# Optimization experiments

Hardware: AMD Instinct MI355X
Metric: run time of the kernel (lower is better)

The kernel has to match this reference:

```python
import jax, jax.numpy as jnp
import numpy as np

# PSLoss constants (from init_kwargs)
MSE_WEIGHT = 0.5
W_CORR = 1.0
W_VAR = 1.0
W_MEAN = 1.0
K = 3           # k_dominant_freqs
MIN_PATCH = 5   # min_patch_len (max(2, 5))
EPS = 1e-8


def setup_inputs() -> dict:
    key = jax.random.key(0)
    k1, k2 = jax.random.split(key)
    B, T, F = 64, 336, 321
    forecast = jax.random.normal(k1, (B, T, F), dtype=jnp.float32)
    target = jax.random.normal(k2, (B, T, F), dtype=jnp.float32)
    return {"forecast": forecast, "target": target}


def _structural_loss(fc, tg):
    """fc, tg: [N, T] flattened (batch*features) series. Returns (total_loss_sum, patch_count)."""
    N, T = tg.shape
    Mmax = T // MIN_PATCH  # max segments per period (period >= MIN_PATCH)

    # --- Fourier adaptive patching (vectorized over all N series) ---
    amp = jnp.abs(jnp.fft.rfft(tg, axis=-1))[:, 1:]           # drop DC, [N, T//2]
    _, rel = jax.lax.top_k(amp, K)                             # [N, K]
    freq_idx = (rel + 1).astype(jnp.float32)
    p = jnp.floor(T / freq_idx).astype(jnp.int32)              # dominant periods [N, K]
    # dedup periods in topk order (the original 'processed_periods' set)
    eq = p[:, :, None] == p[:, None, :]                        # [N, K, K]
    earlier = jnp.tril(jnp.ones((K, K), dtype=bool), -1)       # j < k
    dup = jnp.any(eq & earlier, axis=-1)
    valid_p = (p >= MIN_PATCH) & ~dup                          # [N, K]

    nseg = T // p                                              # [N, K] (p >= 2 always)
    s_idx = jnp.arange(Mmax, dtype=jnp.int32)
    seg_s = p[:, :, None] * s_idx                              # [N, K, Mmax]
    seg_e = seg_s + p[:, :, None]
    seg_v = (s_idx < nseg[:, :, None]) & valid_p[:, :, None]
    rem_s = nseg * p                                           # remaining tail patch
    rem_v = valid_p & ((T - rem_s) >= MIN_PATCH)

    starts = jnp.concatenate([seg_s.reshape(N, -1), rem_s], axis=-1)
    ends = jnp.concatenate([seg_e.reshape(N, -1), jnp.full_like(rem_s, T)], axis=-1)
    valid = jnp.concatenate([seg_v.reshape(N, -1), rem_v], axis=-1)
    # fallback whole-series patch if no patch survived
    none = ~jnp.any(valid, axis=-1, keepdims=True)
    starts = jnp.concatenate([starts, jnp.zeros((N, 1), jnp.int32)], axis=-1)
    ends = jnp.concatenate([ends, jnp.full((N, 1), T, jnp.int32)], axis=-1)
    valid = jnp.concatenate([valid, none], axis=-1)            # [N, M]

    # --- dedup identical (start, end) patches (original list(set(...))) ---
    SENT = (T + 1) * (T + 1)
    keys = jnp.where(valid, starts * (T + 1) + ends, SENT)
    keys = jnp.sort(keys, axis=-1)
    uniq = jnp.concatenate(
        [jnp.ones((N, 1), dtype=bool), keys[:, 1:] != keys[:, :-1]], axis=-1)
    valid = (keys != SENT) & uniq
    s = jnp.where(valid, keys // (T + 1), 0)                   # safe dummy (0,2) when invalid
    e = jnp.where(valid, keys % (T + 1), 2)

    # --- per-patch stats via inclusive prefix sums ---
    def csum(x):
        return jnp.concatenate([jnp.zeros((N, 1), x.dtype), jnp.cumsum(x, axis=-1)], axis=-1)

    cs_t, cs_f = csum(tg), csum(fc)
    cs_tt, cs_ff, cs_tf = csum(tg * tg), csum(fc * fc), csum(tg * fc)

    def seg_sum(cs):
        return jnp.take_along_axis(cs, e, axis=-1) - jnp.take_along_axis(cs, s, axis=-1)

    n = (e - s).astype(jnp.float32)
    St, Sf = seg_sum(cs_t), seg_sum(cs_f)
    Stt, Sff, Stf = seg_sum(cs_tt), seg_sum(cs_ff), seg_sum(cs_tf)
    mt, mf = St / n, Sf / n
    tvs = jnp.maximum(Stt - n * mt * mt, 0.0)   # sum of squared deviations (target)
    fvs = jnp.maximum(Sff - n * mf * mf, 0.0)
    num = Stf - n * mt * mf
    corr = num / (jnp.sqrt(tvs * fvs) + EPS)
    corr_loss = 1.0 - jnp.abs(corr)
    tvar = tvs / (n - 1.0)                      # torch.var is unbiased
    fvar = fvs / (n - 1.0)
    var_loss = jnp.abs(tvar - fvar) / (tvar + EPS)
    mean_loss = jnp.abs(mt - mf) / (jnp.abs(mt) + EPS)
    patch_loss = W_CORR * corr_loss + W_VAR * var_loss + W_MEAN * mean_loss

    total = jnp.sum(jnp.where(valid, patch_loss, 0.0))
    count = jnp.sum(valid)
    return total, count


def reference(forecast, target):
    B, T, F = forecast.shape
    fc = jnp.transpose(forecast, (0, 2, 1)).reshape(B * F, T)
    tg = jnp.transpose(target, (0, 2, 1)).reshape(B * F, T)
    total, count = _structural_loss(fc, tg)
    avg = jnp.where(count > 0,
                    total / jnp.maximum(count, 1).astype(jnp.float32),
                    jnp.float32(0.0))
    mse = jnp.mean((forecast - target) ** 2)
    return MSE_WEIGHT * mse + (1.0 - MSE_WEIGHT) * avg
```

## Files before the change

kernel.cpp:

```cpp
#include <hip/hip_runtime.h>
#include <hip/hip_bf16.h>

#define TT 336
#define NF 321
#define NB 64
#define NSER (NB * NF)
#define WPB 4
#define KP 352
#define LDA 360
#define SPP 16
#define WV 8
#define NFB (NSER / SPP)
#define NFBG 1288
#define TSP 340

#define TWS 1056

#define TGX 11
#define TGY 11
#define NMSEP (TGX * TGY * NB)

typedef __attribute__((ext_vector_type(8))) short bf16x8;
typedef __attribute__((ext_vector_type(4))) float f32x4;
typedef unsigned long long ULL;

__device__ __forceinline__ unsigned short f2bf(float v) {
    unsigned x = __float_as_uint(v);
    x += 0x7FFFu + ((x >> 16) & 1u);
    return (unsigned short)(x >> 16);
}

__device__ __forceinline__ void ins3(ULL& a0, ULL& a1, ULL& a2, ULL x) {
    ULL hi = a0 > x ? a0 : x;
    ULL lo = a0 > x ? x : a0;
    a0 = hi;
    ULL hi1 = a1 > lo ? a1 : lo;
    ULL lo1 = a1 > lo ? lo : a1;
    a1 = hi1;
    a2 = a2 > lo1 ? a2 : lo1;
}

__device__ __forceinline__ int idiv336(int d) {
    return (int)(__fdividef(336.0f, (float)d));
}

__global__ void twiddle_k(unsigned short* __restrict__ Wb) {
    int n = blockIdx.x;
    int f = (n >> 1) + 1;
    int isSin = n & 1;
    for (int k = threadIdx.x; k < KP; k += blockDim.x) {
        float v = 0.0f;
        if (k < TT) {
            int r = (f * k) % TT;
            float ang = 6.2831853071795864769f * (float)r / 336.0f;
            v = isSin ? sinf(ang) : cosf(ang);
        }
        Wb[(size_t)n * KP + k] = f2bf(v);
    }
}

__device__ __forceinline__ float patch_loss_f32(float S1, float S2, float S3,
                                                float S4, float S5, int n) {
    float nnf = (float)n;
    float invf = 1.0f / nnf;
    float tvs = S3 - S1 * S1 * invf; tvs = tvs > 0.f ? tvs : 0.f;
    float fvs = S4 - S2 * S2 * invf; fvs = fvs > 0.f ? fvs : 0.f;
    float num = S5 - S1 * S2 * invf;
    float corr = num / (sqrtf(tvs * fvs) + 1e-8f);
    float closs = 1.0f - fabsf(corr);
    float vloss = fabsf(tvs - fvs) / (tvs + (nnf - 1.0f) * 1e-8f);
    float mloss = fabsf(S1 - S2) / (fabsf(S1) + nnf * 1e-8f);
    return closs + vloss + mloss;
}

__device__ __forceinline__ double patch_loss(double S1, double S2, double S3,
                                             double S4, double S5, double nn) {
    double mt = S1 / nn, mf = S2 / nn;
    double tvs = S3 - nn * mt * mt; tvs = tvs > 0.0 ? tvs : 0.0;
    double fvs = S4 - nn * mf * mf; fvs = fvs > 0.0 ? fvs : 0.0;
    double num = S5 - nn * mt * mf;
    double corr = num / (sqrt(tvs * fvs) + 1e-8);
    double closs = 1.0 - fabs(corr);
    double tvar = tvs / (nn - 1.0), fvar = fvs / (nn - 1.0);
    double vloss = fabs(tvar - fvar) / (tvar + 1e-8);
    double mloss = fabs(mt - mf) / (fabs(mt) + 1e-8);
    return closs + vloss + mloss;
}

struct PatchCfg {
    int P[3], nseg[3], rs[3];
    float rp[3];
    bool vp[3], hr[3];
};

__device__ __forceinline__ void make_cfg(int fr0, int fr1, int fr2, PatchCfg& c) {
    c.P[0] = idiv336(fr0); c.P[1] = idiv336(fr1); c.P[2] = idiv336(fr2);
    c.vp[0] = (c.P[0] >= 5);
    c.vp[1] = (c.P[1] >= 5) && (c.P[1] != c.P[0]);
    c.vp[2] = (c.P[2] >= 5) && (c.P[2] != c.P[0]) && (c.P[2] != c.P[1]);
#pragma unroll
    for (int q = 0; q < 3; q++) {
        c.nseg[q] = idiv336(c.P[q] > 0 ? c.P[q] : 1);
        c.rs[q] = c.nseg[q] * c.P[q];
        c.hr[q] = c.vp[q] && ((TT - c.rs[q]) >= 5);
        c.rp[q] = (c.P[q] > 0) ? __frcp_rn((float)c.P[q]) : 0.0f;
    }
}

__device__ __forceinline__ bool slot_patch(const PatchCfg& c, int i, int& s, int& e) {
    bool kept = false;
    s = 0; e = 0;
    if (i < 204) {
        int k = (i >= 136) ? 2 : ((i >= 68) ? 1 : 0);
        int si = i - k * 68;
        if (c.vp[k]) {
            if (si < c.nseg[k]) { s = c.P[k] * si; e = s + c.P[k]; kept = true; }
            else if (si == c.nseg[k] && c.hr[k]) { s = c.rs[k]; e = TT; kept = true; }
            if (kept) {
#pragma unroll
                for (int j = 0; j < 2; j++) {
                    if (j < k && c.vp[j]) {
                        bool dup = (s == c.rs[j]) && (e == TT) && c.hr[j];
                        int len = e - s;
                        if (len == c.P[j] && s < c.rs[j] && (s % c.P[j]) == 0) dup = true;
                        if (dup) kept = false;
                    }
                }
            }
        }
    }
    return kept;
}

__global__ __launch_bounds__(512) void fused_k(const float* __restrict__ tgO,
                                               const float* __restrict__ fcO,
                                               const unsigned short* __restrict__ Wb,
                                               double* __restrict__ blkout) {
    __shared__ __align__(16) char smem[43520 + WV * TWS * 4];
    float2* ts = (float2*)smem;
    unsigned short* sA = (unsigned short*)(smem + 43520);
    ULL* tk3 = (ULL*)(smem + 43520 + 11520);
    float* tabAll = (float*)(smem + 43520);
    __shared__ uint4 tkf[SPP];
    __shared__ double wms[WV], wls[WV];
    __shared__ int wlc[WV];

    const int tid = threadIdx.x;
    const int wave = tid >> 6, lane = tid & 63;
    const int lb = (blockIdx.x & 7) * 161 + (blockIdx.x >> 3);
    if (lb >= NFB) return;
    const int serBase = lb * SPP;

    const int j = tid & 15, tch = tid >> 4;
    int t0, nT;
    if (tch < 16) { t0 = tch * 11; nT = 11; }
    else          { t0 = 176 + (tch - 16) * 10; nT = 10; }
    float va[11], vc[11];
    {
        const int ser = serBase + j;
        const int bb = ser / NF, ff = ser - bb * NF;
        const float* tb_ = tgO + (size_t)bb * TT * NF + ff;
        const float* fb_ = fcO + (size_t)bb * TT * NF + ff;
#pragma unroll
        for (int i = 0; i < 11; i++) if (i < nT) va[i] = tb_[(size_t)(t0 + i) * NF];
#pragma unroll
        for (int i = 0; i < 11; i++) if (i < nT) vc[i] = fb_[(size_t)(t0 + i) * NF];
#pragma unroll
        for (int i = 0; i < 11; i++) {
            if (i < nT) sA[j * LDA + (t0 + i)] = f2bf(va[i]);
        }
        if (tid < SPP * 16) sA[(tid & 15) * LDA + TT + (tid >> 4)] = 0;
    }
    __syncthreads();

    const int quad = lane >> 4, c = lane & 15;
    ULL t0k[4] = {0, 0, 0, 0}, t1k[4] = {0, 0, 0, 0}, t2k[4] = {0, 0, 0, 0};
    {
        const unsigned short* aRow = sA + c * LDA + quad * 8;
        const int ntStart = (wave < 5) ? wave * 3 : 15 + (wave - 5) * 2;
        const int ntEnd = ntStart + ((wave < 5) ? 3 : 2);

        for (int nt = ntStart; nt < ntEnd; nt++) {
            const unsigned short* bRow = Wb + (size_t)(nt * 16 + c) * KP + quad * 8;
            f32x4 acc = (f32x4){0.f, 0.f, 0.f, 0.f};
#pragma unroll
            for (int ks = 0; ks < 11; ks++) {
                bf16x8 a = *(const bf16x8*)(aRow + ks * 32);
                bf16x8 b = *(const bf16x8*)(bRow + ks * 32);
                acc = __builtin_amdgcn_mfma_f32_16x16x32_bf16(a, b, acc, 0, 0, 0);
            }
            int n = nt * 16 + c;
            unsigned fidx = (unsigned)((n >> 1) + 1);
            unsigned ftag = 0xFFFFFFFFu - fidx;
            bool odd = (n & 1) != 0;
#pragma unroll
            for (int r = 0; r < 4; r++) {
                float v = acc[r];
                float p = v * v;
                p += __shfl_xor(p, 1, 64);
                ULL key = odd ? 0ull
                              : (((ULL)__float_as_uint(p) << 32) | (ULL)ftag);
                ins3(t0k[r], t1k[r], t2k[r], key);
            }
        }
#pragma unroll
        for (int m = 2; m <= 8; m <<= 1) {
#pragma unroll
            for (int r = 0; r < 4; r++) {
                ULL b0 = __shfl_xor(t0k[r], m, 64);
                ULL b1 = __shfl_xor(t1k[r], m, 64);
                ULL b2 = __shfl_xor(t2k[r], m, 64);
                ins3(t0k[r], t1k[r], t2k[r], b0);
                ins3(t0k[r], t1k[r], t2k[r], b1);
                ins3(t0k[r], t1k[r], t2k[r], b2);
            }
        }
    }

    {
        float ms = 0.0f;
#pragma unroll
        for (int i = 0; i < 11; i++) {
            if (i < nT) {
                int t = t0 + i;
                ts[j * TSP + t] = make_float2(va[i], vc[i]);
                float d = va[i] - vc[i];
                ms = fmaf(d, d, ms);
            }
        }
        for (int off = 32; off; off >>= 1) ms += __shfl_down(ms, off, 64);
        if (lane == 0) wms[wave] = (double)ms;
    }

    if (c == 0) {
#pragma unroll
        for (int r = 0; r < 4; r++) {
            int s = quad * 4 + r;
            tk3[(wave * 16 + s) * 3 + 0] = t0k[r];
            tk3[(wave * 16 + s) * 3 + 1] = t1k[r];
            tk3[(wave * 16 + s) * 3 + 2] = t2k[r];
        }
    }
    __syncthreads();
    if (tid < SPP) {
        ULL k0 = 0, k1 = 0, k2 = 0;
#pragma unroll
        for (int wv = 0; wv < WV; wv++) {
#pragma unroll
            for (int jj = 0; jj < 3; jj++) ins3(k0, k1, k2, tk3[(wv * 16 + tid) * 3 + jj]);
        }
        unsigned f0 = 0xFFFFFFFFu - (unsigned)(k0 & 0xFFFFFFFFull);
        unsigned f1 = 0xFFFFFFFFu - (unsigned)(k1 & 0xFFFFFFFFull);
        unsigned f2 = 0xFFFFFFFFu - (unsigned)(k2 & 0xFFFFFFFFull);
        tkf[tid] = make_uint4(f0, f1, f2, 0u);
    }
    __syncthreads();

    float* tw = tabAll + wave * TWS;
    float lsum = 0.0f;
    int lcnt = 0;
#pragma unroll 1
    for (int r = 0; r < 2; r++) {
        const int jj = (wave << 1) | r;

        uint4 tk = tkf[jj];
        PatchCfg cfg;
        make_cfg((int)tk.x, (int)tk.y, (int)tk.z, cfg);

        float2 loc[6];
        float c1 = 0.f, c2 = 0.f, c3 = 0.f, c4 = 0.f, c5 = 0.f;
        if (lane < 56) {
            const float4* lp = (const float4*)(ts + jj * TSP + 6 * lane);
            float4 fa = lp[0], fb = lp[1], fcc = lp[2];
            loc[0] = make_float2(fa.x, fa.y); loc[1] = make_float2(fa.z, fa.w);
            loc[2] = make_float2(fb.x, fb.y); loc[3] = make_float2(fb.z, fb.w);
            loc[4] = make_float2(fcc.x, fcc.y); loc[5] = make_float2(fcc.z, fcc.w);
#pragma unroll
            for (int i = 0; i < 6; i++) {
                float a = loc[i].x, b = loc[i].y;
                c1 += a; c2 += b;
                c3 = fmaf(a, a, c3); c4 = fmaf(b, b, c4); c5 = fmaf(a, b, c5);
            }
        }

        float s1 = c1, s2 = c2, s3 = c3, s4 = c4, s5 = c5;
#pragma unroll
        for (int off = 1; off < 64; off <<= 1) {
            float y1 = __shfl_up(s1, off, 64);
            float y2 = __shfl_up(s2, off, 64);
            float y3 = __shfl_up(s3, off, 64);
            float y4 = __shfl_up(s4, off, 64);
            float y5 = __shfl_up(s5, off, 64);
            if (lane >= off) { s1 += y1; s2 += y2; s3 += y3; s4 += y4; s5 += y5; }
        }

        if (lane == 63) {
#pragma unroll
            for (int k = 0; k < 3; k++) {
#pragma unroll
                for (int q = 0; q < 5; q++) tw[(k * 70) * 5 + q] = 0.f;
            }
        }
        if (lane < 56) {
            float r1 = s1 - c1, r2 = s2 - c2;
            float r3 = s3 - c3, r4 = s4 - c4, r5 = s5 - c5;
#pragma unroll
            for (int i = 0; i < 6; i++) {
                float a = loc[i].x, b = loc[i].y;
                r1 += a; r2 += b;
                r3 = fmaf(a, a, r3); r4 = fmaf(b, b, r4); r5 = fmaf(a, b, r5);
                int tp = 6 * lane + i + 1;
                float tpf = (float)tp;
                if (tp == TT) {
                    tw[1050] = r1; tw[1051] = r2; tw[1052] = r3;
                    tw[1053] = r4; tw[1054] = r5;
                }
#pragma unroll
                for (int k = 0; k < 3; k++) {
                    if (cfg.vp[k]) {
                        int q = (int)(tpf * cfg.rp[k] + 0.001f);
                        if (q * cfg.P[k] == tp && q <= 68) {
                            int ix = (k * 70 + q) * 5;
                            tw[ix + 0] = r1; tw[ix + 1] = r2; tw[ix + 2] = r3;
                            tw[ix + 3] = r4; tw[ix + 4] = r5;
                        }
                    }
                }
            }
        }

        ULL anyMask = 0ull;
#pragma unroll
        for (int rI = 0; rI < 4; rI++) {
            int i = lane + 64 * rI;
            int s, e;
            bool kept = slot_patch(cfg, i, s, e);
            ULL bal = __ballot(kept);
            anyMask |= bal;
            if (bal == 0ull) continue;
            if (kept) {
                int k = (i >= 136) ? 2 : ((i >= 68) ? 1 : 0);
                int si = i - k * 68;
                bool tail = (si == cfg.nseg[k]);
                const float* pS = tw + (k * 70 + si) * 5;
                const float* pE = tail ? (tw + 1050) : (tw + (k * 70 + si + 1) * 5);
                float S1 = pE[0] - pS[0];
                float S2 = pE[1] - pS[1];
                float S3 = pE[2] - pS[2];
                float S4 = pE[3] - pS[3];
                float S5 = pE[4] - pS[4];
                lsum += patch_loss_f32(S1, S2, S3, S4, S5, e - s);
                lcnt += 1;
            }
        }
        if (anyMask == 0ull) {
            if (lane == 0) {
                lsum += patch_loss_f32(tw[1050], tw[1051], tw[1052],
                                       tw[1053], tw[1054], TT);
                lcnt += 1;
            }
        }
    }

    for (int off = 32; off; off >>= 1) {
        lsum += __shfl_down(lsum, off, 64);
        lcnt += __shfl_down(lcnt, off, 64);
    }
    if (lane == 0) { wls[wave] = (double)lsum; wlc[wave] = lcnt; }
    __syncthreads();
    if (tid == 0) {
        double L = 0.0, M = 0.0;
        int C = 0;
#pragma unroll
        for (int wv = 0; wv < WV; wv++) { L += wls[wv]; C += wlc[wv]; M += wms[wv]; }
        blkout[3 * lb + 0] = L;
        blkout[3 * lb + 1] = (double)C;
        blkout[3 * lb + 2] = M;
    }
}

__global__ __launch_bounds__(256) void transpose_k(const float* __restrict__ fc,
                                                   const float* __restrict__ tg,
                                                   float2* __restrict__ out,
                                                   double* __restrict__ msep,
                                                   double* __restrict__ acc) {
    __shared__ float ta[32][33];
    __shared__ float tb[32][33];
    __shared__ double wacc[4];
    const int b = blockIdx.z;
    const int t0 = blockIdx.x * 32, f0 = blockIdx.y * 32;
    const int tx = threadIdx.x, ty = threadIdx.y;
    const size_t base = (size_t)b * TT * NF;
    double ms = 0.0;
#pragma unroll
    for (int k = 0; k < 4; k++) {
        int t = t0 + ty + 8 * k, f = f0 + tx;
        if (t < TT && f < NF) {
            float a = tg[base + (size_t)t * NF + f];
            float c = fc[base + (size_t)t * NF + f];
            ta[ty + 8 * k][tx] = a;
            tb[ty + 8 * k][tx] = c;
            double d = (double)a - (double)c;
            ms += d * d;
        }
    }
    __syncthreads();
#pragma unroll
    for (int k = 0; k < 4; k++) {
        int f = f0 + ty + 8 * k, t = t0 + tx;
        if (t < TT && f < NF) {
            out[((size_t)b * NF + f) * TT + t] =
                make_float2(ta[tx][ty + 8 * k], tb[tx][ty + 8 * k]);
        }
    }
    for (int off = 32; off; off >>= 1) ms += __shfl_down(ms, off, 64);
    int flat = ty * 32 + tx;
    int lane = flat & 63, wid = flat >> 6;
    if (lane == 0) wacc[wid] = ms;
    __syncthreads();
    if (flat == 0) {
        double tot = wacc[0] + wacc[1] + wacc[2] + wacc[3];
        if (msep) {
            int blk = (blockIdx.z * TGY + blockIdx.y) * TGX + blockIdx.x;
            msep[blk] = tot;
        } else {
            atomicAdd(&acc[0], tot);
        }
    }
}

__global__ void mse_k(const float* __restrict__ fc, const float* __restrict__ tg,
                      double* __restrict__ acc) {
    const size_t N4 = (size_t)NB * TT * NF / 4;
    const float4* a4 = (const float4*)fc;
    const float4* b4 = (const float4*)tg;
    double s = 0.0;
    for (size_t i = (size_t)blockIdx.x * blockDim.x + threadIdx.x; i < N4;
         i += (size_t)gridDim.x * blockDim.x) {
        float4 a = a4[i], b = b4[i];
        double d0 = (double)a.x - (double)b.x;
        double d1 = (double)a.y - (double)b.y;
        double d2 = (double)a.z - (double)b.z;
        double d3 = (double)a.w - (double)b.w;
        s += d0 * d0 + d1 * d1 + d2 * d2 + d3 * d3;
    }
    for (int off = 32; off; off >>= 1) s += __shfl_down(s, off, 64);
    __shared__ double wsum[4];
    int flat = threadIdx.x;
    int lane = flat & 63, wid = flat >> 6;
    if (lane == 0) wsum[wid] = s;
    __syncthreads();
    if (flat == 0) atomicAdd(&acc[0], wsum[0] + wsum[1] + wsum[2] + wsum[3]);
}

__device__ __forceinline__ void patch_body(const float2* tsw, int lane,
                                           int fr0, int fr1, int fr2,
                                           double& lsum, double& lcnt) {
    PatchCfg cfg;
    make_cfg(fr0, fr1, fr2, cfg);
    ULL anyMask = 0ull;
#pragma unroll
    for (int rI = 0; rI < 4; rI++) {
        int s, e;
        bool kept = slot_patch(cfg, lane + 64 * rI, s, e);
        anyMask |= __ballot(kept);
        if (kept) {
            double S1 = 0, S2 = 0, S3 = 0, S4 = 0, S5 = 0;
            for (int t = s; t < e; t++) {
                float2 v = tsw[t];
                double a = (double)v.x, b = (double)v.y;
                S1 += a; S2 += b;
                S3 += a * a; S4 += b * b; S5 += a * b;
            }
            lsum += patch_loss(S1, S2, S3, S4, S5, (double)(e - s));
            lcnt += 1.0;
        }
    }
    if (anyMask == 0ull) {
        double S1 = 0, S2 = 0, S3 = 0, S4 = 0, S5 = 0;
        for (int t = lane; t < TT; t += 64) {
            float2 v = tsw[t];
            double a = (double)v.x, b = (double)v.y;
            S1 += a; S2 += b;
            S3 += a * a; S4 += b * b; S5 += a * b;
        }
        for (int off = 32; off; off >>= 1) {
            S1 += __shfl_down(S1, off, 64);
            S2 += __shfl_down(S2, off, 64);
            S3 += __shfl_down(S3, off, 64);
            S4 += __shfl_down(S4, off, 64);
            S5 += __shfl_down(S5, off, 64);
        }
        if (lane == 0) {
            lsum += patch_loss(S1, S2, S3, S4, S5, (double)TT);
            lcnt += 1.0;
        }
    }
}

__global__ __launch_bounds__(256, 6) void series_k(const float2* __restrict__ tsG,
                                                   const float* __restrict__ fcG,
                                                   const float* __restrict__ tgG,
                                                   int transposed,
                                                   double2* __restrict__ pairs,
                                                   double* __restrict__ acc) {
    const int w = threadIdx.x >> 6, lane = threadIdx.x & 63;
    const int ser = blockIdx.x * WPB + w;
    __shared__ float2 ts[WPB][TT];
    __shared__ float4 zb[WPB][84];

    if (transposed) {
        const float2* sp = tsG + (size_t)ser * TT;
        for (int t = lane; t < TT; t += 64) ts[w][t] = sp[t];
    } else {
        int b = ser / NF, f = ser - b * NF;
        const float* tp = tgG + (size_t)b * TT * NF + f;
        const float* fp = fcG + (size_t)b * TT * NF + f;
        for (int t = lane; t < TT; t += 64)
            ts[w][t] = make_float2(tp[(size_t)t * NF], fp[(size_t)t * NF]);
    }
    __syncthreads();

    for (int t = lane; t < 84; t += 64) {
        float x0 = ts[w][t].x, x1 = ts[w][t + 84].x;
        float x2 = ts[w][t + 168].x, x3 = ts[w][t + 252].x;
        float a = x0 + x2, b2 = x1 + x3, c = x0 - x2, d = x1 - x3;
        zb[w][t] = make_float4(a + b2, a - b2, c, d);
    }
    __syncthreads();

    const double TWOPI = 6.283185307179586476925286766559;
    int fb[3] = {1 + lane, 65 + lane, 129 + lane};
    float cc[3], sn[3], re[3], im[3], cd[3], sd[3], sgn[3];
    int selA[3];
#pragma unroll
    for (int q = 0; q < 3; q++) {
        int f = fb[q], cls = f & 3;
        double dl = (double)f * (TWOPI / 336.0);
        cd[q] = (float)cos(dl);
        sd[q] = (float)sin(dl);
        cc[q] = 1.0f; sn[q] = 0.0f; re[q] = 0.0f; im[q] = 0.0f;
        sgn[q] = (cls == 1) ? -1.0f : ((cls == 3) ? 1.0f : 0.0f);
        selA[q] = (cls == 0) ? 0 : ((cls == 2) ? 1 : 2);
    }
    for (int t = 0; t < 84; t++) {
        float4 zv = zb[w][t];
#pragma unroll
        for (int q = 0; q < 3; q++) {
            float zr = (selA[q] == 0) ? zv.x : ((selA[q] == 1) ? zv.y : zv.z);
            float zi = sgn[q] * zv.w;
            re[q] = fmaf(zr, cc[q], re[q]);
            re[q] = fmaf(zi, sn[q], re[q]);
            im[q] = fmaf(zi, cc[q], im[q]);
            im[q] = fmaf(-zr, sn[q], im[q]);
            float nc = fmaf(cc[q], cd[q], -(sn[q] * sd[q]));
            float ns = fmaf(sn[q], cd[q], cc[q] * sd[q]);
            cc[q] = nc; sn[q] = ns;
        }
    }

    ULL k0 = 0, k1 = 0, k2 = 0;
#pragma unroll
    for (int q = 0; q < 3; q++) {
        float a2 = fmaf(re[q], re[q], im[q] * im[q]);
        ULL key = ((ULL)__float_as_uint(a2) << 32) |
                  (ULL)(0xFFFFFFFFu - (unsigned)fb[q]);
        if (fb[q] > 168) key = 0ull;
        ins3(k0, k1, k2, key);
    }
    for (int m = 1; m < 64; m <<= 1) {
        ULL b0 = __shfl_xor(k0, m, 64);
        ULL b1 = __shfl_xor(k1, m, 64);
        ULL b2 = __shfl_xor(k2, m, 64);
        ins3(k0, k1, k2, b0); ins3(k0, k1, k2, b1); ins3(k0, k1, k2, b2);
    }

    int fr0 = (int)(0xFFFFFFFFu - (unsigned)(k0 & 0xFFFFFFFFull));
    int fr1 = (int)(0xFFFFFFFFu - (unsigned)(k1 & 0xFFFFFFFFull));
    int fr2 = (int)(0xFFFFFFFFu - (unsigned)(k2 & 0xFFFFFFFFull));

    double lsum = 0.0, lcnt = 0.0;
    patch_body(&ts[w][0], lane, fr0, fr1, fr2, lsum, lcnt);

    for (int off = 32; off; off >>= 1) {
        lsum += __shfl_down(lsum, off, 64);
        lcnt += __shfl_down(lcnt, off, 64);
    }
    if (lane == 0) {
        if (pairs) {
            pairs[ser] = make_double2(lsum, lcnt);
        } else {
            atomicAdd(&acc[1], lsum);
            atomicAdd(&acc[2], lcnt);
        }
    }
}

__global__ __launch_bounds__(1024) void reduce3_k(const double* __restrict__ blkout,
                                                  float* __restrict__ out) {
    const int tid = threadIdx.x;
    double ls = 0.0, lc = 0.0, ms = 0.0;
    for (int i = tid; i < NFB; i += 1024) {
        ls += blkout[3 * i + 0];
        lc += blkout[3 * i + 1];
        ms += blkout[3 * i + 2];
    }
    for (int off = 32; off; off >>= 1) {
        ls += __shfl_down(ls, off, 64);
        lc += __shfl_down(lc, off, 64);
        ms += __shfl_down(ms, off, 64);
    }
    __shared__ double sl[16], sc[16], sm[16];
    int lane = tid & 63, wid = tid >> 6;
    if (lane == 0) { sl[wid] = ls; sc[wid] = lc; sm[wid] = ms; }
    __syncthreads();
    if (tid == 0) {
        double L = 0, C = 0, M = 0;
        for (int i = 0; i < 16; i++) { L += sl[i]; C += sc[i]; M += sm[i]; }
        double mse = M / (double)((size_t)NB * TT * NF);
        double avg = (C > 0.0) ? (L / C) : 0.0;
        out[0] = (float)(0.5 * mse + 0.5 * avg);
    }
}

__global__ __launch_bounds__(1024) void reduce_k(const double2* __restrict__ pairs,
                                                 const double* __restrict__ msep,
                                                 int nmse,
                                                 float* __restrict__ out) {
    const int tid = threadIdx.x;
    double ls = 0.0, lc = 0.0, ms = 0.0;
    for (int i = tid; i < NSER; i += 1024) {
        double2 p = pairs[i];
        ls += p.x; lc += p.y;
    }
    for (int i = tid; i < nmse; i += 1024) ms += msep[i];
    for (int off = 32; off; off >>= 1) {
        ls += __shfl_down(ls, off, 64);
        lc += __shfl_down(lc, off, 64);
        ms += __shfl_down(ms, off, 64);
    }
    __shared__ double sl[16], sc[16], sm[16];
    int lane = tid & 63, wid = tid >> 6;
    if (lane == 0) { sl[wid] = ls; sc[wid] = lc; sm[wid] = ms; }
    __syncthreads();
    if (tid == 0) {
        double L = 0, C = 0, M = 0;
        for (int i = 0; i < 16; i++) { L += sl[i]; C += sc[i]; M += sm[i]; }
        double mse = M / (double)((size_t)NB * TT * NF);
        double avg = (C > 0.0) ? (L / C) : 0.0;
        out[0] = (float)(0.5 * mse + 0.5 * avg);
    }
}

__global__ void finalize_k(const double* __restrict__ acc, float* __restrict__ out) {
    double mse = acc[0] / (double)((size_t)NB * TT * NF);
    double avg = (acc[2] > 0.0) ? (acc[1] / acc[2]) : 0.0;
    out[0] = (float)(0.5 * mse + 0.5 * avg);
}

extern "C" void kernel_launch(void* const* d_in, const int* in_sizes, int n_in,
                              void* d_out, int out_size, void* d_ws, size_t ws_size,
                              hipStream_t stream) {
    const float* fc = (const float*)d_in[0];
    const float* tg = (const float*)d_in[1];
    float* out = (float*)d_out;
    char* ws = (char*)d_ws;
    double* acc = (double*)ws;

    const size_t OFF_MSE = 64;
    const size_t OFF_PAIR = OFF_MSE + (size_t)NMSEP * sizeof(double);
    const size_t OFF_TOP = OFF_PAIR + (size_t)NSER * sizeof(double2);
    const size_t OFF_W = OFF_TOP + (size_t)NSER * sizeof(uint4);
    const size_t OFF_END2 = OFF_W + (size_t)TT * KP * sizeof(unsigned short);
    const size_t bytesT = (size_t)NSER * TT * sizeof(float2);
    const bool big2 = (ws_size >= OFF_END2);
    const size_t R3_OFF_TS = OFF_PAIR + (size_t)NSER * sizeof(double2);
    const bool big = !big2 && (ws_size >= R3_OFF_TS + bytesT);
    const bool mid = !big2 && !big && (ws_size >= OFF_MSE + bytesT);

    double* msep = (double*)(ws + OFF_MSE);
    double* blkout = (double*)(ws + OFF_PAIR);
    unsigned short* Wb = (unsigned short*)(ws + OFF_W);

    dim3 tg_grid(TGX, TGY, NB);
    dim3 tg_blk(32, 8);

    if (big2) {
        twiddle_k<<<TT, 128, 0, stream>>>(Wb);
        fused_k<<<NFBG, 64 * WV, 0, stream>>>(tg, fc, Wb, blkout);
        reduce3_k<<<1, 1024, 0, stream>>>(blkout, out);
    } else if (big) {
        float2* tsT = (float2*)(ws + R3_OFF_TS);
        transpose_k<<<tg_grid, tg_blk, 0, stream>>>(fc, tg, tsT, msep, acc);
        series_k<<<NSER / WPB, 64 * WPB, 0, stream>>>(tsT, fc, tg, 1,
                                                      (double2*)blkout, acc);
        reduce_k<<<1, 1024, 0, stream>>>((double2*)blkout, msep, NMSEP, out);
    } else if (mid) {
        float2* tsT = (float2*)(ws + OFF_MSE);
        hipMemsetAsync(d_ws, 0, 64, stream);
        transpose_k<<<tg_grid, tg_blk, 0, stream>>>(fc, tg, tsT, nullptr, acc);
        series_k<<<NSER / WPB, 64 * WPB, 0, stream>>>(tsT, fc, tg, 1, nullptr, acc);
        finalize_k<<<1, 1, 0, stream>>>(acc, out);
    } else {
        hipMemsetAsync(d_ws, 0, 64, stream);
        mse_k<<<1024, 256, 0, stream>>>(fc, tg, acc);
        series_k<<<NSER / WPB, 64 * WPB, 0, stream>>>(nullptr, fc, tg, 0, nullptr, acc);
        finalize_k<<<1, 1, 0, stream>>>(acc, out);
    }
}
```

Before: 152.1 us.

## Reuse series tile smem for per-period prefix tables to cut LDS footprint

Removes the separate per-wave 1056-float prefix table region and instead overlays a smaller per-period table on the shared series buffer, processing the three dominant periods one at a time. Tail totals are taken by shuffling from lane 55 instead of being stored in LDS, and the top-k staging writes plus barrier move before the MSE accumulation. The aim is lower LDS use per block, so more blocks can be resident at once. In exchange it adds a sequential per-period loop with extra ballots and writes over a shared buffer that other waves may still be reading, and it depends on the layout of the table overlay being correct.

```diff
diff --git a/kernel.cpp b/kernel.cpp
--- a/kernel.cpp
+++ b/kernel.cpp
@@ -14,8 +14,6 @@
 #define NFBG 1288
 #define TSP 340
 
-#define TWS 1056
-
 #define TGX 11
 #define TGY 11
 #define NMSEP (TGX * TGY * NB)
@@ -136,11 +134,10 @@
                                                const float* __restrict__ fcO,
                                                const unsigned short* __restrict__ Wb,
                                                double* __restrict__ blkout) {
-    __shared__ __align__(16) char smem[43520 + WV * TWS * 4];
+    __shared__ __align__(16) char smem[43520 + 3072];
     float2* ts = (float2*)smem;
-    unsigned short* sA = (unsigned short*)(smem + 43520);
-    ULL* tk3 = (ULL*)(smem + 43520 + 11520);
-    float* tabAll = (float*)(smem + 43520);
+    unsigned short* sA = (unsigned short*)smem;
+    ULL* tk3 = (ULL*)(smem + 43520);
     __shared__ uint4 tkf[SPP];
     __shared__ double wms[WV], wls[WV];
     __shared__ int wlc[WV];
@@ -216,6 +213,16 @@
             }
         }
     }
+    if (c == 0) {
+#pragma unroll
+        for (int r = 0; r < 4; r++) {
+            int s = quad * 4 + r;
+            tk3[(wave * 16 + s) * 3 + 0] = t0k[r];
+            tk3[(wave * 16 + s) * 3 + 1] = t1k[r];
+            tk3[(wave * 16 + s) * 3 + 2] = t2k[r];
+        }
+    }
+    __syncthreads();
 
     {
         float ms = 0.0f;
@@ -231,17 +238,6 @@
         for (int off = 32; off; off >>= 1) ms += __shfl_down(ms, off, 64);
         if (lane == 0) wms[wave] = (double)ms;
     }
-
-    if (c == 0) {
-#pragma unroll
-        for (int r = 0; r < 4; r++) {
-            int s = quad * 4 + r;
-            tk3[(wave * 16 + s) * 3 + 0] = t0k[r];
-            tk3[(wave * 16 + s) * 3 + 1] = t1k[r];
-            tk3[(wave * 16 + s) * 3 + 2] = t2k[r];
-        }
-    }
-    __syncthreads();
     if (tid < SPP) {
         ULL k0 = 0, k1 = 0, k2 = 0;
 #pragma unroll
@@ -256,7 +252,7 @@
     }
     __syncthreads();
 
-    float* tw = tabAll + wave * TWS;
+    float* tw = (float*)smem + (size_t)(wave * 2) * (TSP * 2);
     float lsum = 0.0f;
     int lcnt = 0;
 #pragma unroll 1
@@ -294,69 +290,82 @@
             if (lane >= off) { s1 += y1; s2 += y2; s3 += y3; s4 += y4; s5 += y5; }
         }
 
-        if (lane == 63) {
-#pragma unroll
-            for (int k = 0; k < 3; k++) {
-#pragma unroll
-                for (int q = 0; q < 5; q++) tw[(k * 70) * 5 + q] = 0.f;
-            }
-        }
-        if (lane < 56) {
-            float r1 = s1 - c1, r2 = s2 - c2;
-            float r3 = s3 - c3, r4 = s4 - c4, r5 = s5 - c5;
-#pragma unroll
-            for (int i = 0; i < 6; i++) {
-                float a = loc[i].x, b = loc[i].y;
-                r1 += a; r2 += b;
-                r3 = fmaf(a, a, r3); r4 = fmaf(b, b, r4); r5 = fmaf(a, b, r5);
-                int tp = 6 * lane + i + 1;
-                float tpf = (float)tp;
-                if (tp == TT) {
-                    tw[1050] = r1; tw[1051] = r2; tw[1052] = r3;
-                    tw[1053] = r4; tw[1054] = r5;
+        float T1 = __shfl(s1, 55, 64);
+        float T2 = __shfl(s2, 55, 64);
+        float T3 = __shfl(s3, 55, 64);
+        float T4 = __shfl(s4, 55, 64);
+        float T5 = __shfl(s5, 55, 64);
+
+        ULL anyMask = 0ull;
+#pragma unroll 1
+        for (int k = 0; k < 3; k++) {
+            if (!cfg.vp[k]) continue;
+            if (lane == 63) {
+#pragma unroll
+                for (int q = 0; q < 5; q++) tw[q] = 0.f;
+            }
+            if (lane < 56) {
+                float r1 = s1 - c1, r2 = s2 - c2;
+                float r3 = s3 - c3, r4 = s4 - c4, r5 = s5 - c5;
+#pragma unroll
+                for (int i = 0; i < 6; i++) {
+                    float a = loc[i].x, b = loc[i].y;
+                    r1 += a; r2 += b;
+                    r3 = fmaf(a, a, r3); r4 = fmaf(b, b, r4); r5 = fmaf(a, b, r5);
+                    int tp = 6 * lane + i + 1;
+                    int q = (int)((float)tp * cfg.rp[k] + 0.001f);
+                    if (q * cfg.P[k] == tp && q <= 68) {
+                        int ix = q * 5;
+                        tw[ix + 0] = r1; tw[ix + 1] = r2; tw[ix + 2] = r3;
+                        tw[ix + 3] = r4; tw[ix + 4] = r5;
+                    }
                 }
-#pragma unroll
-                for (int k = 0; k < 3; k++) {
-                    if (cfg.vp[k]) {
-                        int q = (int)(tpf * cfg.rp[k] + 0.001f);
-                        if (q * cfg.P[k] == tp && q <= 68) {
-                            int ix = (k * 70 + q) * 5;
-                            tw[ix + 0] = r1; tw[ix + 1] = r2; tw[ix + 2] = r3;
-                            tw[ix + 3] = r4; tw[ix + 4] = r5;
+            }
+
+#pragma unroll 1
+            for (int rI = 0; rI < 2; rI++) {
+                int si = lane + 64 * rI;
+                bool kept = false;
+                int s = 0, e = 0;
+                if (si < cfg.nseg[k]) { s = cfg.P[k] * si; e = s + cfg.P[k]; kept = true; }
+                else if (si == cfg.nseg[k] && cfg.hr[k]) { s = cfg.rs[k]; e = TT; kept = true; }
+                if (kept) {
+#pragma unroll
+                    for (int jd = 0; jd < 2; jd++) {
+                        if (jd < k && cfg.vp[jd]) {
+                            bool dup = (s == cfg.rs[jd]) && (e == TT) && cfg.hr[jd];
+                            int len = e - s;
+                            int qq = (int)((float)s * cfg.rp[jd] + 0.001f);
+                            if (len == cfg.P[jd] && s < cfg.rs[jd] &&
+                                qq * cfg.P[jd] == s) dup = true;
+                            if (dup) kept = false;
                         }
                     }
                 }
-            }
-        }
-
-        ULL anyMask = 0ull;
-#pragma unroll
-        for (int rI = 0; rI < 4; rI++) {
-            int i = lane + 64 * rI;
-            int s, e;
-            bool kept = slot_patch(cfg, i, s, e);
-            ULL bal = __ballot(kept);
-            anyMask |= bal;
-            if (bal == 0ull) continue;
-            if (kept) {
-                int k = (i >= 136) ? 2 : ((i >= 68) ? 1 : 0);
-                int si = i - k * 68;
-                bool tail = (si == cfg.nseg[k]);
-                const float* pS = tw + (k * 70 + si) * 5;
-                const float* pE = tail ? (tw + 1050) : (tw + (k * 70 + si + 1) * 5);
-                float S1 = pE[0] - pS[0];
-                float S2 = pE[1] - pS[1];
-                float S3 = pE[2] - pS[2];
-                float S4 = pE[3] - pS[3];
-                float S5 = pE[4] - pS[4];
-                lsum += patch_loss_f32(S1, S2, S3, S4, S5, e - s);
-                lcnt += 1;
+                ULL bal = __ballot(kept);
+                anyMask |= bal;
+                if (bal == 0ull) continue;
+                if (kept) {
+                    bool tail = (si == cfg.nseg[k]);
+                    const float* pS = tw + si * 5;
+                    float S1, S2, S3, S4, S5;
+                    if (tail) {
+                        S1 = T1 - pS[0]; S2 = T2 - pS[1]; S3 = T3 - pS[2];
+                        S4 = T4 - pS[3]; S5 = T5 - pS[4];
+                    } else {
+                        const float* pE = tw + (si + 1) * 5;
+                        S1 = pE[0] - pS[0]; S2 = pE[1] - pS[1];
+                        S3 = pE[2] - pS[2]; S4 = pE[3] - pS[3];
+                        S5 = pE[4] - pS[4];
+                    }
+                    lsum += patch_loss_f32(S1, S2, S3, S4, S5, e - s);
+                    lcnt += 1;
+                }
             }
         }
         if (anyMask == 0ull) {
             if (lane == 0) {
-                lsum += patch_loss_f32(tw[1050], tw[1051], tw[1052],
-                                       tw[1053], tw[1054], TT);
+                lsum += patch_loss_f32(T1, T2, T3, T4, T5, TT);
                 lcnt += 1;
             }
         }
```

Measured after the change: 169.2 us. 11.2% more time.
